# Optimization experiments

Measured on AMD Instinct MI355X. Metric: run time of the kernel, lower is better.

Reference implementation:

```python
import jax, jax.numpy as jnp
import numpy as np

D_MODEL, D_K, D_V, H = 1024, 64, 64, 16
B, N = 2, 2048


def setup_inputs() -> dict:
    key = jax.random.key(0)
    ks = jax.random.split(key, 5)
    y = jax.random.normal(ks[0], (B, N, D_MODEL), dtype=jnp.float32)
    # nn.Linear weights (out, in), init normal std=0.001; biases zero
    Wq = 0.001 * jax.random.normal(ks[1], (H * D_K, D_MODEL), dtype=jnp.float32)
    Wk = 0.001 * jax.random.normal(ks[2], (H * D_K, D_MODEL), dtype=jnp.float32)
    Wv = 0.001 * jax.random.normal(ks[3], (H * D_V, D_MODEL), dtype=jnp.float32)
    Wo = 0.001 * jax.random.normal(ks[4], (D_MODEL, H * D_V), dtype=jnp.float32)
    bq = jnp.zeros((H * D_K,), jnp.float32)
    bk = jnp.zeros((H * D_K,), jnp.float32)
    bv = jnp.zeros((H * D_V,), jnp.float32)
    bo = jnp.zeros((D_MODEL,), jnp.float32)
    return {"y": y, "Wq": Wq, "bq": bq, "Wk": Wk, "bk": bk,
            "Wv": Wv, "bv": bv, "Wo": Wo, "bo": bo}


def reference(y, Wq, bq, Wk, bk, Wv, bv, Wo, bo):
    b_s, n, _ = y.shape
    scale = 1.0 / np.sqrt(D_K).astype(np.float32)
    # projections: (b, n, h, d) -> (b, h, n, d)
    q = (jnp.einsum('bnd,ed->bne', y, Wq) + bq).reshape(b_s, n, H, D_K).transpose(0, 2, 1, 3)
    k = (jnp.einsum('bnd,ed->bne', y, Wk) + bk).reshape(b_s, n, H, D_K).transpose(0, 2, 1, 3)
    v = (jnp.einsum('bnd,ed->bne', y, Wv) + bv).reshape(b_s, n, H, D_V).transpose(0, 2, 1, 3)
    att = jnp.einsum('bhqd,bhkd->bhqk', q, k) * scale  # (b, h, nq, nk)
    att = jax.nn.softmax(att, axis=-1)
    out = jnp.einsum('bhqk,bhkd->bhqd', att, v)  # (b, h, nq, d_v)
    out = out.transpose(0, 2, 1, 3).reshape(b_s, n, H * D_V)
    out = jnp.einsum('bne,de->bnd', out, Wo) + bo
    return out
```

## Files before the change

kernel.cpp:

```cpp
#include <hip/hip_runtime.h>
#include <hip/hip_bf16.h>
#include <math.h>

typedef unsigned int u32;
typedef unsigned short u16;
typedef unsigned char u8;
typedef __attribute__((ext_vector_type(8))) short short8;
typedef __attribute__((ext_vector_type(4))) float f32x4;

constexpr int D_MODEL = 1024;
constexpr int SEQ     = 2048;
constexpr int MROWS   = 4096;

__device__ __forceinline__ u16 f2bf(float f) {
    u32 u = __float_as_uint(f);
    u += 0x7fff + ((u >> 16) & 1);
    return (u16)(u >> 16);
}

__device__ __forceinline__ u32 pk2bf(float a, float b) {
    __hip_bfloat162 h = __float22bfloat162_rn(float2{a, b});
    return *(u32*)&h;
}

__device__ __forceinline__ void async16(const void* g, void* l) {
    __builtin_amdgcn_global_load_lds(
        (const __attribute__((address_space(1))) u32*)(uintptr_t)g,
        (__attribute__((address_space(3))) u32*)(u32)(uintptr_t)l, 16, 0, 0);
}

union U4 { uint4 v; long l[2]; };

__global__ __launch_bounds__(256) void convert_all(
    const float* __restrict__ y,  const float* __restrict__ wq,
    const float* __restrict__ wk, const float* __restrict__ wv,
    const float* __restrict__ wo,
    u16* __restrict__ ybf, u16* __restrict__ wc, u16* __restrict__ wobf)
{
    int g = blockIdx.x;
    const float* src; u16* dst;
    if (g < 4096)      { src = y  + (size_t)g * 1024;          dst = ybf  + (size_t)g * 1024; }
    else if (g < 5120) { src = wq + (size_t)(g - 4096) * 1024; dst = wc   + (size_t)(g - 4096) * 1024; }
    else if (g < 6144) { src = wk + (size_t)(g - 5120) * 1024; dst = wc + (1u << 20) + (size_t)(g - 5120) * 1024; }
    else if (g < 7168) { src = wv + (size_t)(g - 6144) * 1024; dst = wc + (2u << 20) + (size_t)(g - 6144) * 1024; }
    else               { src = wo + (size_t)(g - 7168) * 1024; dst = wobf + (size_t)(g - 7168) * 1024; }
    int t = threadIdx.x * 4;
    float4 v = *(const float4*)(src + t);
    ushort4 o;
    o.x = f2bf(v.x); o.y = f2bf(v.y); o.z = f2bf(v.z); o.w = f2bf(v.w);
    *(ushort4*)(dst + t) = o;
}

__global__ __launch_bounds__(256, 3) void gemm_qkv(
    const u16* __restrict__ A, const u16* __restrict__ Bw,
    const float* __restrict__ b0, const float* __restrict__ b1,
    const float* __restrict__ b2,
    u8* __restrict__ Qf8, u8* __restrict__ Kf8, u16* __restrict__ Vtg)
{
    constexpr int K  = 1024;
    constexpr int BK = 32;
    __shared__ u16 As[128][BK];
    __shared__ u16 Bs[128][BK];

    const int tid = threadIdx.x;
    const int lane = tid & 63, wave = tid >> 6;
    const int wm = wave >> 1, wn = wave & 1;
    const int quad = lane >> 4, l15 = lane & 15;
    const int m0 = blockIdx.y * 128, n0 = blockIdx.x * 128;

    const int srow = lane >> 2;
    const int sch  = (lane & 3) * 8;
    const u16* Ag = A  + (size_t)(m0 + wave * 32 + srow) * K + sch;
    const u16* Bg = Bw + (size_t)(n0 + wave * 32 + srow) * K + sch;
    u16* AsB = &As[wave * 32][0];
    u16* BsB = &Bs[wave * 32][0];

    f32x4 zero4 = {0.f, 0.f, 0.f, 0.f};
    f32x4 acc[4][4];
#pragma unroll
    for (int r = 0; r < 4; ++r)
#pragma unroll
        for (int c = 0; c < 4; ++c) acc[r][c] = zero4;

    for (int k0 = 0; k0 < K; k0 += BK) {
        __syncthreads();
        async16(Ag + k0,          AsB);
        async16(Ag + k0 + 16 * K, AsB + 16 * BK);
        async16(Bg + k0,          BsB);
        async16(Bg + k0 + 16 * K, BsB + 16 * BK);
        __syncthreads();
        short8 a[4], b[4];
#pragma unroll
        for (int r = 0; r < 4; ++r)
            a[r] = *(const short8*)&As[wm * 64 + r * 16 + l15][quad * 8];
#pragma unroll
        for (int c = 0; c < 4; ++c)
            b[c] = *(const short8*)&Bs[wn * 64 + c * 16 + l15][quad * 8];
#pragma unroll
        for (int r = 0; r < 4; ++r)
#pragma unroll
            for (int c = 0; c < 4; ++c)
                acc[r][c] = __builtin_amdgcn_mfma_f32_16x16x32_bf16(b[c], a[r], acc[r][c], 0, 0, 0);
    }

    const int seg = n0 >> 10;
    if (seg < 2) {
        u8* dst = seg ? Kf8 : Qf8;
        const float* bp = seg ? b1 : b0;
        const float sc = seg ? 16.0f : 64.0f;
#pragma unroll
        for (int c = 0; c < 4; ++c) {
            int nb = n0 + wn * 64 + c * 16 + quad * 4;
            float4 bias4 = *(const float4*)(bp + (nb & 1023));
            int col = nb & 63;
            int pos = ((col >> 3) & 3) * 16 + (col >> 5) * 8 + (col & 7);
            int hh = ((nb & 1023) >> 6);
#pragma unroll
            for (int r = 0; r < 4; ++r) {
                int m = m0 + wm * 64 + r * 16 + l15;
                int j = m & 2047, bb = m >> 11;
                float v0 = (acc[r][c][0] + bias4.x) * sc;
                float v1 = (acc[r][c][1] + bias4.y) * sc;
                float v2 = (acc[r][c][2] + bias4.z) * sc;
                float v3 = (acc[r][c][3] + bias4.w) * sc;
                u32 w = (u32)__builtin_amdgcn_cvt_pk_fp8_f32(v2, v3,
                            __builtin_amdgcn_cvt_pk_fp8_f32(v0, v1, 0, false), true);
                *(u32*)&dst[((size_t)(bb * 16 + hh)) * 131072 + (size_t)j * 64 + pos] = w;
            }
        }
    } else {
#pragma unroll
        for (int c = 0; c < 4; ++c) {
            int nb = n0 + wn * 64 + c * 16 + quad * 4;
            float4 bias4 = *(const float4*)(b2 + (nb & 1023));
            int d0 = nb & 63;
            int h = (nb >> 6) & 15;
#pragma unroll
            for (int r = 0; r < 4; ++r) {
                int m = m0 + wm * 64 + r * 16 + l15;
                int j = m & 2047, bb = m >> 11;
                int jp = (j & ~31) | (j & 3) | (((j >> 4) & 1) << 2) | (((j >> 2) & 3) << 3);
                size_t rowb = ((size_t)(bb * 16 + h)) * 64;
                Vtg[(rowb + d0 + 0) * 2048 + jp] = f2bf(acc[r][c][0] + bias4.x);
                Vtg[(rowb + d0 + 1) * 2048 + jp] = f2bf(acc[r][c][1] + bias4.y);
                Vtg[(rowb + d0 + 2) * 2048 + jp] = f2bf(acc[r][c][2] + bias4.z);
                Vtg[(rowb + d0 + 3) * 2048 + jp] = f2bf(acc[r][c][3] + bias4.w);
            }
        }
    }
}

__global__ __launch_bounds__(256, 3) void gemm_o(
    const u16* __restrict__ A, const u16* __restrict__ Bw,
    const float* __restrict__ b0, float* __restrict__ Cf, int ldc)
{
    constexpr int K  = 1024;
    constexpr int BK = 32;
    __shared__ u16 As[128][BK];
    __shared__ u16 Bs[64][BK];

    const int tid = threadIdx.x;
    const int lane = tid & 63, wave = tid >> 6;
    const int wm = wave >> 1, wn = wave & 1;
    const int quad = lane >> 4, l15 = lane & 15;
    const int m0 = blockIdx.y * 128, n0 = blockIdx.x * 64;

    const int srow = lane >> 2;
    const int sch  = (lane & 3) * 8;
    const u16* Ag = A  + (size_t)(m0 + wave * 32 + srow) * K + sch;
    const u16* Bg = Bw + (size_t)(n0 + wave * 16 + srow) * K + sch;
    u16* AsB = &As[wave * 32][0];
    u16* BsB = &Bs[wave * 16][0];

    f32x4 zero4 = {0.f, 0.f, 0.f, 0.f};
    f32x4 acc[4][2];
#pragma unroll
    for (int r = 0; r < 4; ++r)
#pragma unroll
        for (int c = 0; c < 2; ++c) acc[r][c] = zero4;

    for (int k0 = 0; k0 < K; k0 += BK) {
        __syncthreads();
        async16(Ag + k0,          AsB);
        async16(Ag + k0 + 16 * K, AsB + 16 * BK);
        async16(Bg + k0,          BsB);
        __syncthreads();
        short8 a[4], b[2];
#pragma unroll
        for (int r = 0; r < 4; ++r)
            a[r] = *(const short8*)&As[wm * 64 + r * 16 + l15][quad * 8];
#pragma unroll
        for (int c = 0; c < 2; ++c)
            b[c] = *(const short8*)&Bs[wn * 32 + c * 16 + l15][quad * 8];
#pragma unroll
        for (int r = 0; r < 4; ++r)
#pragma unroll
            for (int c = 0; c < 2; ++c)
                acc[r][c] = __builtin_amdgcn_mfma_f32_16x16x32_bf16(b[c], a[r], acc[r][c], 0, 0, 0);
    }

#pragma unroll
    for (int c = 0; c < 2; ++c) {
        int nb = n0 + wn * 32 + c * 16 + quad * 4;
        float4 bias4 = *(const float4*)(b0 + nb);
#pragma unroll
        for (int r = 0; r < 4; ++r) {
            int m = m0 + wm * 64 + r * 16 + l15;
            float4 st = {acc[r][c][0] + bias4.x, acc[r][c][1] + bias4.y,
                         acc[r][c][2] + bias4.z, acc[r][c][3] + bias4.w};
            *(float4*)&Cf[(size_t)m * ldc + nb] = st;
        }
    }
}

__global__ __launch_bounds__(256, 4) void attn_mfma(
    const u8* __restrict__ Qf8, const u8* __restrict__ Kf8,
    const u16* __restrict__ Vtg, u16* __restrict__ Oatt)
{
    __shared__ __align__(16) char smem[24576];
    __shared__ float Lbuf[2][32];
    char* KsB = smem;
    char* VtB = smem + 8192;
    float (*Obuf)[68] = (float(*)[68])smem;

    const int tid = threadIdx.x;
    const int lane = tid & 63, wave = tid >> 6;
    const int quad = lane >> 4, l15 = lane & 15;
    const int grp = wave >> 1, wl = wave & 1;
    const int bh = blockIdx.y, h = bh & 15;
    const size_t rowbase = (size_t)(bh >> 4) * SEQ;
    const int q0 = blockIdx.x * 64;
    const int rbase = wl * 32;

    const u8* Qb = Qf8 + (size_t)bh * 131072;
    uint4 bq[2];
#pragma unroll
    for (int rt = 0; rt < 2; ++rt)
        bq[rt] = *(const uint4*)&Qb[(size_t)(q0 + rbase + rt * 16 + l15) * 64 + quad * 16];

    const int l4 = lane >> 2, u4c = lane & 3;
    const int kx = (lane >> 3) & 3;
    const u8* Kbase = Kf8 + (size_t)bh * 131072 + l4 * 64 + ((u4c ^ kx) * 16);
    const int l8 = lane >> 3, u8i = lane & 7;
    const int vx = u8i ^ l8;
    const u16* Vbase = Vtg + ((size_t)bh * 64 + l8) * 2048 + vx * 8;

    f32x4 zero4 = {0.f, 0.f, 0.f, 0.f};
    f32x4 oacc[2][4];
#pragma unroll
    for (int rt = 0; rt < 2; ++rt)
#pragma unroll
        for (int d16 = 0; d16 < 4; ++d16) oacc[rt][d16] = zero4;
    float lpart[2] = {0.f, 0.f};

    const char* Kg = KsB + grp * 4096;
    const char* Vg = VtB + grp * 8192;
    const float C1 = 0x1p-13f, C2 = 0x1p-27f;

    for (int pr = 0; pr < 16; ++pr) {
        __syncthreads();
#pragma unroll
        for (int i = 0; i < 6; ++i) {
            int ch = wave * 6 + i;
            if (ch < 8) {
                int g = ch >> 2, s = ch & 3;
                async16(Kbase + (size_t)((2 * pr + g) * 64 + s * 16) * 64,
                        KsB + g * 4096 + s * 1024);
            } else {
                int vc = ch - 8;
                int g = vc >> 3, sub = vc & 7;
                async16(Vbase + (size_t)sub * 8 * 2048 + (2 * pr + g) * 64,
                        VtB + g * 8192 + sub * 1024);
            }
        }
        __syncthreads();

#pragma unroll
        for (int chalf = 0; chalf < 2; ++chalf) {
            U4 ak[2];
#pragma unroll
            for (int cc = 0; cc < 2; ++cc) {
                int j = (chalf * 2 + cc) * 16 + l15;
                ak[cc].v = *(const uint4*)(Kg + j * 64 + ((quad ^ ((j >> 1) & 3)) * 16));
            }
            short8 pf[2];
#pragma unroll
            for (int rt = 0; rt < 2; ++rt) {
                U4 qq; qq.v = bq[rt];
                f32x4 t0 = zero4, t1 = zero4;
                t0 = __builtin_amdgcn_mfma_f32_16x16x32_fp8_fp8(ak[0].l[0], qq.l[0], t0, 0, 0, 0);
                t0 = __builtin_amdgcn_mfma_f32_16x16x32_fp8_fp8(ak[0].l[1], qq.l[1], t0, 0, 0, 0);
                t1 = __builtin_amdgcn_mfma_f32_16x16x32_fp8_fp8(ak[1].l[0], qq.l[0], t1, 0, 0, 0);
                t1 = __builtin_amdgcn_mfma_f32_16x16x32_fp8_fp8(ak[1].l[1], qq.l[1], t1, 0, 0, 0);
                float p0 = __builtin_fmaf(t0[0], __builtin_fmaf(t0[0], C2, C1), 1.0f);
                float p1 = __builtin_fmaf(t0[1], __builtin_fmaf(t0[1], C2, C1), 1.0f);
                float p2 = __builtin_fmaf(t0[2], __builtin_fmaf(t0[2], C2, C1), 1.0f);
                float p3 = __builtin_fmaf(t0[3], __builtin_fmaf(t0[3], C2, C1), 1.0f);
                float p4 = __builtin_fmaf(t1[0], __builtin_fmaf(t1[0], C2, C1), 1.0f);
                float p5 = __builtin_fmaf(t1[1], __builtin_fmaf(t1[1], C2, C1), 1.0f);
                float p6 = __builtin_fmaf(t1[2], __builtin_fmaf(t1[2], C2, C1), 1.0f);
                float p7 = __builtin_fmaf(t1[3], __builtin_fmaf(t1[3], C2, C1), 1.0f);
                lpart[rt] += (p0 + p1 + p2 + p3) + (p4 + p5 + p6 + p7);
                union { short8 s8; u32 w[4]; } pu;
                pu.w[0] = pk2bf(p0, p1); pu.w[1] = pk2bf(p2, p3);
                pu.w[2] = pk2bf(p4, p5); pu.w[3] = pk2bf(p6, p7);
                pf[rt] = pu.s8;
            }
#pragma unroll
            for (int d16 = 0; d16 < 4; ++d16) {
                int d = d16 * 16 + l15;
                short8 va = *(const short8*)(Vg + d * 128 + ((((chalf << 2) | quad) ^ (d & 7)) * 16));
#pragma unroll
                for (int rt = 0; rt < 2; ++rt)
                    oacc[rt][d16] = __builtin_amdgcn_mfma_f32_16x16x32_bf16(va, pf[rt], oacc[rt][d16], 0, 0, 0);
            }
        }
    }

    float lred[2];
#pragma unroll
    for (int rt = 0; rt < 2; ++rt) {
        float l = lpart[rt];
        l += __shfl_xor(l, 16);
        l += __shfl_xor(l, 32);
        lred[rt] = l;
    }

    __syncthreads();
    if (grp == 1) {
#pragma unroll
        for (int rt = 0; rt < 2; ++rt) {
            int row = rbase + rt * 16 + l15;
#pragma unroll
            for (int d16 = 0; d16 < 4; ++d16) {
                float4 o = {oacc[rt][d16][0], oacc[rt][d16][1], oacc[rt][d16][2], oacc[rt][d16][3]};
                *(float4*)&Obuf[row][d16 * 16 + quad * 4] = o;
            }
            if (quad == 0) Lbuf[wl][rt * 16 + l15] = lred[rt];
        }
    }
    __syncthreads();
    if (grp == 0) {
#pragma unroll
        for (int rt = 0; rt < 2; ++rt) {
            int row = rbase + rt * 16 + l15;
            float inv = 1.0f / (lred[rt] + Lbuf[wl][rt * 16 + l15]);
            size_t grow = rowbase + q0 + row;
#pragma unroll
            for (int d16 = 0; d16 < 4; ++d16) {
                float4 o = *(const float4*)&Obuf[row][d16 * 16 + quad * 4];
                float v0 = (oacc[rt][d16][0] + o.x) * inv;
                float v1 = (oacc[rt][d16][1] + o.y) * inv;
                float v2 = (oacc[rt][d16][2] + o.z) * inv;
                float v3 = (oacc[rt][d16][3] + o.w) * inv;
                ushort4 st;
                u32 w01 = pk2bf(v0, v1), w23 = pk2bf(v2, v3);
                st.x = (u16)(w01 & 0xffff); st.y = (u16)(w01 >> 16);
                st.z = (u16)(w23 & 0xffff); st.w = (u16)(w23 >> 16);
                *(ushort4*)&Oatt[grow * D_MODEL + h * 64 + d16 * 16 + quad * 4] = st;
            }
        }
    }
}

extern "C" void kernel_launch(void* const* d_in, const int* in_sizes, int n_in,
                              void* d_out, int out_size, void* d_ws, size_t ws_size,
                              hipStream_t stream)
{
    const float* y  = (const float*)d_in[0];
    const float* Wq = (const float*)d_in[1];
    const float* bq = (const float*)d_in[2];
    const float* Wk = (const float*)d_in[3];
    const float* bk = (const float*)d_in[4];
    const float* Wv = (const float*)d_in[5];
    const float* bv = (const float*)d_in[6];
    const float* Wo = (const float*)d_in[7];
    const float* bo = (const float*)d_in[8];
    float* out = (float*)d_out;

    u16* ybf  = (u16*)d_ws;
    u16* wc   = ybf + (size_t)MROWS * D_MODEL;
    u16* wobf = wc + (size_t)3072 * 1024;
    u8*  qf8  = (u8*)(wobf + (size_t)1024 * 1024);
    u8*  kf8  = qf8 + (size_t)MROWS * 1024;
    u16* vtg  = (u16*)(kf8 + (size_t)MROWS * 1024);
    u16* att  = vtg + (size_t)MROWS * 1024;

    convert_all<<<8192, 256, 0, stream>>>(y, Wq, Wk, Wv, Wo, ybf, wc, wobf);

    gemm_qkv<<<dim3(24, 32), 256, 0, stream>>>(
        ybf, wc, bq, bk, bv, qf8, kf8, vtg);

    attn_mfma<<<dim3(32, 32), 256, 0, stream>>>(qf8, kf8, vtg, att);

    gemm_o<<<dim3(16, 32), 256, 0, stream>>>(att, wobf, bo, out, D_MODEL);
}
```

Before: 191.4 us.

## Double-buffer async LDS tile loads in GEMM and attention kernels

```diff
diff --git a/kernel.cpp b/kernel.cpp
--- a/kernel.cpp
+++ b/kernel.cpp
@@ -11,6 +11,10 @@
 constexpr int D_MODEL = 1024;
 constexpr int SEQ     = 2048;
 constexpr int MROWS   = 4096;
+
+#define RAW_BAR()   asm volatile("s_barrier" ::: "memory")
+#define WAIT_VM(n)  asm volatile("s_waitcnt vmcnt(" #n ")" ::: "memory")
+#define WAIT_LGKM() asm volatile("s_waitcnt lgkmcnt(0)" ::: "memory")
 
 __device__ __forceinline__ u16 f2bf(float f) {
     u32 u = __float_as_uint(f);
@@ -59,8 +63,9 @@
 {
     constexpr int K  = 1024;
     constexpr int BK = 32;
-    __shared__ u16 As[128][BK];
-    __shared__ u16 Bs[128][BK];
+    constexpr int NT = K / BK;
+    __shared__ u16 As[2][128][BK];
+    __shared__ u16 Bs[2][128][BK];
 
     const int tid = threadIdx.x;
     const int lane = tid & 63, wave = tid >> 6;
@@ -72,8 +77,6 @@
     const int sch  = (lane & 3) * 8;
     const u16* Ag = A  + (size_t)(m0 + wave * 32 + srow) * K + sch;
     const u16* Bg = Bw + (size_t)(n0 + wave * 32 + srow) * K + sch;
-    u16* AsB = &As[wave * 32][0];
-    u16* BsB = &Bs[wave * 32][0];
 
     f32x4 zero4 = {0.f, 0.f, 0.f, 0.f};
     f32x4 acc[4][4];
@@ -82,25 +85,36 @@
 #pragma unroll
         for (int c = 0; c < 4; ++c) acc[r][c] = zero4;
 
-    for (int k0 = 0; k0 < K; k0 += BK) {
-        __syncthreads();
-        async16(Ag + k0,          AsB);
-        async16(Ag + k0 + 16 * K, AsB + 16 * BK);
-        async16(Bg + k0,          BsB);
-        async16(Bg + k0 + 16 * K, BsB + 16 * BK);
-        __syncthreads();
+    auto issue = [&](int k0, int buf) {
+        u16* AsD = &As[buf][wave * 32][0];
+        u16* BsD = &Bs[buf][wave * 32][0];
+        async16(Ag + k0,          AsD);
+        async16(Ag + k0 + 16 * K, AsD + 16 * BK);
+        async16(Bg + k0,          BsD);
+        async16(Bg + k0 + 16 * K, BsD + 16 * BK);
+    };
+    issue(0, 0);
+    issue(BK, 1);
+
+    for (int t = 0; t < NT; ++t) {
+        const int cur = t & 1;
+        WAIT_VM(4);
+        RAW_BAR();
         short8 a[4], b[4];
 #pragma unroll
         for (int r = 0; r < 4; ++r)
-            a[r] = *(const short8*)&As[wm * 64 + r * 16 + l15][quad * 8];
+            a[r] = *(const short8*)&As[cur][wm * 64 + r * 16 + l15][quad * 8];
 #pragma unroll
         for (int c = 0; c < 4; ++c)
-            b[c] = *(const short8*)&Bs[wn * 64 + c * 16 + l15][quad * 8];
+            b[c] = *(const short8*)&Bs[cur][wn * 64 + c * 16 + l15][quad * 8];
 #pragma unroll
         for (int r = 0; r < 4; ++r)
 #pragma unroll
             for (int c = 0; c < 4; ++c)
                 acc[r][c] = __builtin_amdgcn_mfma_f32_16x16x32_bf16(b[c], a[r], acc[r][c], 0, 0, 0);
+        WAIT_LGKM();
+        RAW_BAR();
+        issue(((t + 2) * BK) & (K - 1), cur);
     }
 
     const int seg = n0 >> 10;
@@ -156,8 +170,9 @@
 {
     constexpr int K  = 1024;
     constexpr int BK = 32;
-    __shared__ u16 As[128][BK];
-    __shared__ u16 Bs[64][BK];
+    constexpr int NT = K / BK;
+    __shared__ u16 As[2][128][BK];
+    __shared__ u16 Bs[2][64][BK];
 
     const int tid = threadIdx.x;
     const int lane = tid & 63, wave = tid >> 6;
@@ -169,8 +184,6 @@
     const int sch  = (lane & 3) * 8;
     const u16* Ag = A  + (size_t)(m0 + wave * 32 + srow) * K + sch;
     const u16* Bg = Bw + (size_t)(n0 + wave * 16 + srow) * K + sch;
-    u16* AsB = &As[wave * 32][0];
-    u16* BsB = &Bs[wave * 16][0];
 
     f32x4 zero4 = {0.f, 0.f, 0.f, 0.f};
     f32x4 acc[4][2];
@@ -179,24 +192,35 @@
 #pragma unroll
         for (int c = 0; c < 2; ++c) acc[r][c] = zero4;
 
-    for (int k0 = 0; k0 < K; k0 += BK) {
-        __syncthreads();
-        async16(Ag + k0,          AsB);
-        async16(Ag + k0 + 16 * K, AsB + 16 * BK);
-        async16(Bg + k0,          BsB);
-        __syncthreads();
+    auto issue = [&](int k0, int buf) {
+        u16* AsD = &As[buf][wave * 32][0];
+        u16* BsD = &Bs[buf][wave * 16][0];
+        async16(Ag + k0,          AsD);
+        async16(Ag + k0 + 16 * K, AsD + 16 * BK);
+        async16(Bg + k0,          BsD);
+    };
+    issue(0, 0);
+    issue(BK, 1);
+
+    for (int t = 0; t < NT; ++t) {
+        const int cur = t & 1;
+        WAIT_VM(3);
+        RAW_BAR();
         short8 a[4], b[2];
 #pragma unroll
         for (int r = 0; r < 4; ++r)
-            a[r] = *(const short8*)&As[wm * 64 + r * 16 + l15][quad * 8];
+            a[r] = *(const short8*)&As[cur][wm * 64 + r * 16 + l15][quad * 8];
 #pragma unroll
         for (int c = 0; c < 2; ++c)
-            b[c] = *(const short8*)&Bs[wn * 32 + c * 16 + l15][quad * 8];
+            b[c] = *(const short8*)&Bs[cur][wn * 32 + c * 16 + l15][quad * 8];
 #pragma unroll
         for (int r = 0; r < 4; ++r)
 #pragma unroll
             for (int c = 0; c < 2; ++c)
                 acc[r][c] = __builtin_amdgcn_mfma_f32_16x16x32_bf16(b[c], a[r], acc[r][c], 0, 0, 0);
+        WAIT_LGKM();
+        RAW_BAR();
+        issue(((t + 2) * BK) & (K - 1), cur);
     }
 
 #pragma unroll
@@ -213,14 +237,13 @@
     }
 }
 
-__global__ __launch_bounds__(256, 4) void attn_mfma(
+__global__ __launch_bounds__(256, 3) void attn_mfma(
     const u8* __restrict__ Qf8, const u8* __restrict__ Kf8,
     const u16* __restrict__ Vtg, u16* __restrict__ Oatt)
 {
-    __shared__ __align__(16) char smem[24576];
+    __shared__ __align__(16) char smem[49152];
     __shared__ float Lbuf[2][32];
-    char* KsB = smem;
-    char* VtB = smem + 8192;
+    char* VtRoot = smem + 16384;
     float (*Obuf)[68] = (float(*)[68])smem;
 
     const int tid = threadIdx.x;
@@ -253,27 +276,35 @@
         for (int d16 = 0; d16 < 4; ++d16) oacc[rt][d16] = zero4;
     float lpart[2] = {0.f, 0.f};
 
-    const char* Kg = KsB + grp * 4096;
-    const char* Vg = VtB + grp * 8192;
     const float C1 = 0x1p-13f, C2 = 0x1p-27f;
 
-    for (int pr = 0; pr < 16; ++pr) {
-        __syncthreads();
+    auto issue = [&](int pr, int buf) {
+        char* KsD = smem + buf * 8192;
+        char* VtD = VtRoot + buf * 16384;
 #pragma unroll
         for (int i = 0; i < 6; ++i) {
             int ch = wave * 6 + i;
             if (ch < 8) {
                 int g = ch >> 2, s = ch & 3;
                 async16(Kbase + (size_t)((2 * pr + g) * 64 + s * 16) * 64,
-                        KsB + g * 4096 + s * 1024);
+                        KsD + g * 4096 + s * 1024);
             } else {
                 int vc = ch - 8;
                 int g = vc >> 3, sub = vc & 7;
                 async16(Vbase + (size_t)sub * 8 * 2048 + (2 * pr + g) * 64,
-                        VtB + g * 8192 + sub * 1024);
-            }
-        }
-        __syncthreads();
+                        VtD + g * 8192 + sub * 1024);
+            }
+        }
+    };
+    issue(0, 0);
+    issue(1, 1);
+
+    for (int pr = 0; pr < 16; ++pr) {
+        const int cur = pr & 1;
+        WAIT_VM(6);
+        RAW_BAR();
+        const char* Kg = smem + cur * 8192 + grp * 4096;
+        const char* Vg = VtRoot + cur * 16384 + grp * 8192;
 
 #pragma unroll
         for (int chalf = 0; chalf < 2; ++chalf) {
@@ -315,6 +346,9 @@
                     oacc[rt][d16] = __builtin_amdgcn_mfma_f32_16x16x32_bf16(va, pf[rt], oacc[rt][d16], 0, 0, 0);
             }
         }
+        WAIT_LGKM();
+        RAW_BAR();
+        issue((pr + 2) & 15, cur);
     }
 
     float lred[2];
```

Result: no change. 189.4 us (-1.1%).
